# Kernel tuning notes

Measured on AMD Instinct MI355X. Metric: run time of the kernel, lower is better.

## Reference

```python
import jax, jax.numpy as jnp
import numpy as np

B, N, M = 2, 2048, 2048
D = 1024          # query_dim == context_dim == inner_dim
H, DH = 16, 64    # heads, dim_head
SCALE = DH ** -0.5


def setup_inputs() -> dict:
    key = jax.random.key(0)
    ks = jax.random.split(key, 7)
    s = 0.02
    return {
        "x": jax.random.normal(ks[0], (B, N, D), jnp.float32),
        "context": jax.random.normal(ks[1], (B, M, D), jnp.float32),
        "Wq": jax.random.normal(ks[2], (D, H * DH), jnp.float32) * s,
        "Wk": jax.random.normal(ks[3], (D, H * DH), jnp.float32) * s,
        "Wv": jax.random.normal(ks[4], (D, H * DH), jnp.float32) * s,
        "Wo": jax.random.normal(ks[5], (H * DH, D), jnp.float32) * s,
        "bo": jax.random.normal(ks[6], (D,), jnp.float32) * s,
    }


def reference(x, context, Wq, Wk, Wv, Wo, bo):
    # Linear projections (bias-free, as in to_q/to_k/to_v)
    q = (x @ Wq).reshape(B, N, H, DH)        # [B,N,H,DH]
    k = (context @ Wk).reshape(B, M, H, DH)  # [B,M,H,DH]
    v = (context @ Wv).reshape(B, M, H, DH)
    # QK^T * scale, softmax over keys, then AV
    sim = jnp.einsum('bnhd,bmhd->bhnm', q, k) * SCALE  # [B,H,N,M]
    attn = jax.nn.softmax(sim, axis=-1)
    out = jnp.einsum('bhnm,bmhd->bnhd', attn, v)       # [B,N,H,DH]
    out = out.reshape(B, N, H * DH)
    return out @ Wo + bo  # to_out Linear; dropout=0 is identity
```

## Files before the change

kernel.cpp:

```cpp
#include <hip/hip_runtime.h>

#define B_  2
#define N_  2048
#define M_  2048
#define D_  1024
#define H_  16
#define DH_ 64

typedef __bf16 bf16x8 __attribute__((ext_vector_type(8)));
typedef __bf16 bf16x4 __attribute__((ext_vector_type(4)));
typedef short  short4v __attribute__((ext_vector_type(4)));
typedef float  f32x4  __attribute__((ext_vector_type(4)));

#define GAS(p) ((__attribute__((address_space(1))) void*)(p))
#define LAS(p) ((__attribute__((address_space(3))) void*)(p))

#define QPRESCALE 0.18033688011112042f

__device__ __forceinline__ unsigned short f2bf(float f) {
    unsigned int u = __builtin_bit_cast(unsigned int, f);
    u += 0x7fffu + ((u >> 16) & 1u);
    return (unsigned short)(u >> 16);
}

__global__ __launch_bounds__(256) void prep(
    const float* __restrict__ x, const float* __restrict__ ctx,
    const float* __restrict__ Wq, const float* __restrict__ Wk,
    const float* __restrict__ Wv, const float* __restrict__ Wo,
    unsigned short* __restrict__ xb, unsigned short* __restrict__ cb,
    unsigned short* __restrict__ WTbase)
{
    if (blockIdx.z == 4) {
        int blk = blockIdx.y * 32 + blockIdx.x;
        int stride = 1024 * 256;
        for (int i = blk * 256 + threadIdx.x; i < 2097152; i += stride) {
            const float4* src; unsigned short* dst; int j;
            if (i < 1048576) { src = (const float4*)x;   dst = xb; j = i; }
            else             { src = (const float4*)ctx; dst = cb; j = i - 1048576; }
            float4 v = src[j];
            ushort4 o = make_ushort4(f2bf(v.x), f2bf(v.y), f2bf(v.z), f2bf(v.w));
            *(ushort4*)(dst + 4*j) = o;
        }
        return;
    }
    const float* W = (blockIdx.z == 0) ? Wq : (blockIdx.z == 1) ? Wk
                    : (blockIdx.z == 2) ? Wv : Wo;
    unsigned short* WT = WTbase + (size_t)blockIdx.z * 1048576;
    __shared__ unsigned short t[32][33];
    int tx = threadIdx.x & 31, ty8 = threadIdx.x >> 5;
    int c = blockIdx.x * 32 + tx;
#pragma unroll
    for (int i = 0; i < 4; ++i) {
        int r = blockIdx.y * 32 + i*8 + ty8;
        t[i*8 + ty8][tx] = f2bf(W[(size_t)r * 1024 + c]);
    }
    __syncthreads();
    int c2 = blockIdx.y * 32 + tx;
#pragma unroll
    for (int i = 0; i < 4; ++i) {
        int r2 = blockIdx.x * 32 + i*8 + ty8;
        WT[(size_t)r2 * 1024 + c2] = t[tx][i*8 + ty8];
    }
}

__global__ __launch_bounds__(256) void gemm128(
    const unsigned short* __restrict__ xb,
    const unsigned short* __restrict__ cb,
    const unsigned short* __restrict__ wT,
    const unsigned short* __restrict__ aoA,
    unsigned short* __restrict__ qkv_out,
    const float* __restrict__ bo,
    float* __restrict__ outF,
    int base_mode)
{
    __shared__ __align__(16) unsigned short As[128*32];
    __shared__ __align__(16) unsigned short Bs[128*32];

    const int mode = base_mode + blockIdx.z;
    const unsigned short* Amat;
    const unsigned short* Bt;
    if (mode == 0)      { Amat = wT;               Bt = xb; }
    else if (mode == 1) { Amat = wT + 1048576;     Bt = cb; }
    else if (mode == 2) { Amat = cb;               Bt = wT + 2*1048576; }
    else                { Amat = wT + 3*1048576;   Bt = aoA; }

    const int tid = threadIdx.x;
    const int w = tid >> 6, l = tid & 63;
    const int quad = l >> 4, l16 = l & 15;
    const int wm = w & 1, wn = w >> 1;
    int row0, col0;
    if (mode == 2) { row0 = blockIdx.x * 128; col0 = blockIdx.y * 128; }
    else           { row0 = blockIdx.y * 128; col0 = blockIdx.x * 128; }

    f32x4 acc[4][4];
#pragma unroll
    for (int i = 0; i < 4; ++i)
#pragma unroll
        for (int j = 0; j < 4; ++j) acc[i][j] = (f32x4){0.f, 0.f, 0.f, 0.f};

    for (int k0 = 0; k0 < 1024; k0 += 32) {
        __syncthreads();
#pragma unroll
        for (int i = 0; i < 2; ++i) {
            int s = i*256 + w*64 + l;
            int m = s >> 2, c = s & 3;
            int cs = c ^ ((m >> 1) & 3);
            __builtin_amdgcn_global_load_lds(
                GAS(Amat + (size_t)(row0 + m)*1024 + k0 + cs*8),
                LAS(As + (i*256 + w*64)*8), 16, 0, 0);
            __builtin_amdgcn_global_load_lds(
                GAS(Bt + (size_t)(col0 + m)*1024 + k0 + cs*8),
                LAS(Bs + (i*256 + w*64)*8), 16, 0, 0);
        }
        __syncthreads();

        bf16x8 af[4], bfr[4];
#pragma unroll
        for (int mt = 0; mt < 4; ++mt) {
            int m = wm*64 + mt*16 + l16;
            af[mt] = *reinterpret_cast<const bf16x8*>(As + m*32 + (quad ^ ((m >> 1) & 3))*8);
            int n = wn*64 + mt*16 + l16;
            bfr[mt] = *reinterpret_cast<const bf16x8*>(Bs + n*32 + (quad ^ ((n >> 1) & 3))*8);
        }
#pragma unroll
        for (int mt = 0; mt < 4; ++mt)
#pragma unroll
            for (int nt = 0; nt < 4; ++nt)
                acc[mt][nt] = __builtin_amdgcn_mfma_f32_16x16x32_bf16(
                    af[mt], bfr[nt], acc[mt][nt], 0, 0, 0);
    }

    if (mode == 3) {
#pragma unroll
        for (int mt = 0; mt < 4; ++mt) {
            int c = row0 + wm*64 + mt*16 + quad*4;
            float4 bv = *(const float4*)(bo + c);
#pragma unroll
            for (int nt = 0; nt < 4; ++nt) {
                int n = col0 + wn*64 + nt*16 + l16;
                float4 ov = make_float4(acc[mt][nt][0] + bv.x, acc[mt][nt][1] + bv.y,
                                        acc[mt][nt][2] + bv.z, acc[mt][nt][3] + bv.w);
                *(float4*)(outF + (size_t)n*1024 + c) = ov;
            }
        }
    } else if (mode == 2) {
#pragma unroll
        for (int mt = 0; mt < 4; ++mt) {
            int gr = row0 + wm*64 + mt*16 + quad*4;
            int b = gr >> 11, nidx = gr & 2047;
#pragma unroll
            for (int nt = 0; nt < 4; ++nt) {
                int col = col0 + wn*64 + nt*16 + l16;
                int h = col >> 6, d = col & 63;
                ushort4 pk = make_ushort4(f2bf(acc[mt][nt][0]), f2bf(acc[mt][nt][1]),
                                          f2bf(acc[mt][nt][2]), f2bf(acc[mt][nt][3]));
                *(ushort4*)(qkv_out + (size_t)2*4194304
                            + (size_t)((b*16 + h)*64 + d)*2048 + nidx) = pk;
            }
        }
    } else {
        const float qs = (mode == 0) ? QPRESCALE : 1.0f;
        unsigned short* obase = qkv_out + (size_t)mode*4194304;
#pragma unroll
        for (int nt = 0; nt < 4; ++nt) {
            int n = col0 + wn*64 + nt*16 + l16;
            int b = n >> 11, nidx = n & 2047;
#pragma unroll
            for (int mt = 0; mt < 4; ++mt) {
                int c = row0 + wm*64 + mt*16 + quad*4;
                int h = c >> 6, d = c & 63;
                ushort4 pkv = make_ushort4(
                    f2bf(acc[mt][nt][0] * qs), f2bf(acc[mt][nt][1] * qs),
                    f2bf(acc[mt][nt][2] * qs), f2bf(acc[mt][nt][3] * qs));
                *(ushort4*)(obase + (size_t)((b*16 + h)*2048 + nidx)*64 + d) = pkv;
            }
        }
    }
}

__global__ __launch_bounds__(256, 2) void flash_attn(
    const unsigned short* __restrict__ qw,
    const unsigned short* __restrict__ kw,
    const unsigned short* __restrict__ vtw,
    unsigned short* __restrict__ ao)
{
    __shared__ __align__(16) unsigned short Tile[2][9216];

    const int tid = threadIdx.x;
    const int w = tid >> 6, l = tid & 63;
    const int quad = l >> 4, l16 = l & 15;
    const int bh = blockIdx.z * H_ + blockIdx.y;
    const int q0 = blockIdx.x * 128 + w * 32;

    int goff[5];
#pragma unroll
    for (int i = 0; i < 5; ++i) {
        int n = i*256 + w*64 + l;
        int m = (n < 576) ? n : n - 576;
        int row = m / 9, c = m % 9;  if (c > 7) c = 7;
        goff[i] = (n < 576) ? row*64 + c*8 : row*2048 + c*8;
    }
    const unsigned short* kbase = kw + (size_t)bh*131072;
    const unsigned short* vbase = vtw + (size_t)bh*131072;

    bf16x8 qf[2][2];
#pragma unroll
    for (int qg = 0; qg < 2; ++qg)
#pragma unroll
        for (int s = 0; s < 2; ++s)
            qf[qg][s] = *reinterpret_cast<const bf16x8*>(
                qw + (size_t)(bh*2048 + q0 + qg*16 + l16)*64 + s*32 + quad*8);

    f32x4 accO[2][4];
#pragma unroll
    for (int qg = 0; qg < 2; ++qg)
#pragma unroll
        for (int td = 0; td < 4; ++td) accO[qg][td] = (f32x4){0.f, 0.f, 0.f, 0.f};
    float lpart[2] = {0.f, 0.f};

    const f32x4 zz = (f32x4){0.f, 0.f, 0.f, 0.f};

    {
#pragma unroll
        for (int i = 0; i < 4; ++i) {
            const unsigned short* bp = (i*4 + w < 9) ? kbase : vbase;
            __builtin_amdgcn_global_load_lds(GAS(bp + goff[i]),
                LAS(&Tile[0][(i*256 + w*64)*8]), 16, 0, 0);
        }
        if (w < 2)
            __builtin_amdgcn_global_load_lds(GAS(vbase + goff[4]),
                LAS(&Tile[0][(1024 + w*64)*8]), 16, 0, 0);
    }

    for (int it = 0; it < 32; ++it) {
        __syncthreads();
        const int cur = it & 1;

        if (it + 1 < 32) {
            const unsigned short* kp = kbase + (it+1)*4096;
            const unsigned short* vp = vbase + (it+1)*64;
#pragma unroll
            for (int i = 0; i < 4; ++i) {
                const unsigned short* bp = (i*4 + w < 9) ? kp : vp;
                __builtin_amdgcn_global_load_lds(GAS(bp + goff[i]),
                    LAS(&Tile[cur^1][(i*256 + w*64)*8]), 16, 0, 0);
            }
            if (w < 2)
                __builtin_amdgcn_global_load_lds(GAS(vp + goff[4]),
                    LAS(&Tile[cur^1][(1024 + w*64)*8]), 16, 0, 0);
        }

        const unsigned short* Ks = &Tile[cur][0];
        const unsigned short* Vs = &Tile[cur][4608];

        f32x4 sac[2][4];
#pragma unroll
        for (int t = 0; t < 4; ++t) {
            const unsigned short* krow = Ks + (t*16 + l16)*72 + quad*8;
            bf16x8 kf0 = *reinterpret_cast<const bf16x8*>(krow);
            bf16x8 kf1 = *reinterpret_cast<const bf16x8*>(krow + 32);
            sac[0][t] = __builtin_amdgcn_mfma_f32_16x16x32_bf16(kf0, qf[0][0], zz, 0, 0, 0);
            sac[1][t] = __builtin_amdgcn_mfma_f32_16x16x32_bf16(kf0, qf[1][0], zz, 0, 0, 0);
            sac[0][t] = __builtin_amdgcn_mfma_f32_16x16x32_bf16(kf1, qf[0][1], sac[0][t], 0, 0, 0);
            sac[1][t] = __builtin_amdgcn_mfma_f32_16x16x32_bf16(kf1, qf[1][1], sac[1][t], 0, 0, 0);
        }

        short4v pk[2][4];
#pragma unroll
        for (int qg = 0; qg < 2; ++qg) {
            float s0 = 0.f, s1 = 0.f, s2 = 0.f, s3 = 0.f;
#pragma unroll
            for (int t = 0; t < 4; ++t) {
                float p0 = __builtin_amdgcn_exp2f(sac[qg][t][0]);
                float p1 = __builtin_amdgcn_exp2f(sac[qg][t][1]);
                float p2 = __builtin_amdgcn_exp2f(sac[qg][t][2]);
                float p3 = __builtin_amdgcn_exp2f(sac[qg][t][3]);
                s0 += p0; s1 += p1; s2 += p2; s3 += p3;
                bf16x4 pb;
                pb[0] = (__bf16)p0; pb[1] = (__bf16)p1;
                pb[2] = (__bf16)p2; pb[3] = (__bf16)p3;
                pk[qg][t] = __builtin_bit_cast(short4v, pb);
            }
            lpart[qg] += (s0 + s1) + (s2 + s3);
        }

#pragma unroll
        for (int td = 0; td < 4; ++td) {
            const unsigned short* vrow = Vs + (td*16 + l16)*72 + quad*4;
#pragma unroll
            for (int t = 0; t < 4; ++t) {
                short4v vf = *reinterpret_cast<const short4v*>(vrow + t*16);
                accO[0][td] = __builtin_amdgcn_mfma_f32_16x16x16bf16_1k(
                    vf, pk[0][t], accO[0][td], 0, 0, 0);
                accO[1][td] = __builtin_amdgcn_mfma_f32_16x16x16bf16_1k(
                    vf, pk[1][t], accO[1][td], 0, 0, 0);
            }
        }
    }

#pragma unroll
    for (int qg = 0; qg < 2; ++qg) {
        float s = lpart[qg];
        s += __shfl_xor(s, 16);
        s += __shfl_xor(s, 32);
        float inv = 1.f / s;
        const size_t rowbase =
            (size_t)(blockIdx.z*2048 + q0 + qg*16 + l16)*1024 + blockIdx.y*64;
#pragma unroll
        for (int td = 0; td < 4; ++td)
#pragma unroll
            for (int r = 0; r < 4; ++r)
                ao[rowbase + td*16 + quad*4 + r] = f2bf(accO[qg][td][r] * inv);
    }
}

extern "C" void kernel_launch(void* const* d_in, const int* in_sizes, int n_in,
                              void* d_out, int out_size, void* d_ws, size_t ws_size,
                              hipStream_t stream)
{
    const float* x   = (const float*)d_in[0];
    const float* ctx = (const float*)d_in[1];
    const float* Wq  = (const float*)d_in[2];
    const float* Wk  = (const float*)d_in[3];
    const float* Wv  = (const float*)d_in[4];
    const float* Wo  = (const float*)d_in[5];
    const float* bo  = (const float*)d_in[6];
    float* out = (float*)d_out;

    unsigned short* ws  = (unsigned short*)d_ws;
    unsigned short* xb  = ws;
    unsigned short* cb  = ws + 4194304;
    unsigned short* wT  = ws + 8388608;
    unsigned short* qkv = ws + 12582912;
    unsigned short* ao  = ws;

    prep<<<dim3(32, 32, 5), dim3(256), 0, stream>>>(x, ctx, Wq, Wk, Wv, Wo, xb, cb, wT);
    gemm128<<<dim3(32, 8, 3), dim3(256), 0, stream>>>(xb, cb, wT, ao, qkv, bo, out, 0);
    flash_attn<<<dim3(16, 16, 2), dim3(256), 0, stream>>>(qkv, qkv + 4194304, qkv + 8388608, ao);
    gemm128<<<dim3(32, 8, 1), dim3(256), 0, stream>>>(xb, cb, wT, ao, qkv, bo, out, 3);
}
```

Measured before the change: 205.3 us.

## Split attention over key halves and merge partial outputs in a separate kernel

The flash attention kernel now splits the 2048 keys into two halves processed by separate blocks. This doubles the grid and raises launch bounds to 4 blocks per CU for better occupancy and latency hiding. Each half writes its unnormalized bf16 output and its row sums. A new merge kernel adds the two halves and normalizes. The cost is an extra launch, extra global traffic for the partials, and a second bf16 rounding of unnormalized values.

```diff
diff --git a/kernel.cpp b/kernel.cpp
--- a/kernel.cpp
+++ b/kernel.cpp
@@ -178,19 +178,22 @@
     }
 }
 
-__global__ __launch_bounds__(256, 2) void flash_attn(
+__global__ __launch_bounds__(256, 4) void flash_attn(
     const unsigned short* __restrict__ qw,
     const unsigned short* __restrict__ kw,
     const unsigned short* __restrict__ vtw,
-    unsigned short* __restrict__ ao)
+    unsigned short* __restrict__ oh,
+    float* __restrict__ ls)
 {
     __shared__ __align__(16) unsigned short Tile[2][9216];
 
     const int tid = threadIdx.x;
     const int w = tid >> 6, l = tid & 63;
     const int quad = l >> 4, l16 = l & 15;
-    const int bh = blockIdx.z * H_ + blockIdx.y;
+    const int b = blockIdx.z >> 1, half = blockIdx.z & 1;
+    const int bh = b * H_ + blockIdx.y;
     const int q0 = blockIdx.x * 128 + w * 32;
+    const int it0 = half * 16;
 
     int goff[5];
 #pragma unroll
@@ -221,22 +224,24 @@
     const f32x4 zz = (f32x4){0.f, 0.f, 0.f, 0.f};
 
     {
+        const unsigned short* kp = kbase + it0*4096;
+        const unsigned short* vp = vbase + it0*64;
 #pragma unroll
         for (int i = 0; i < 4; ++i) {
-            const unsigned short* bp = (i*4 + w < 9) ? kbase : vbase;
+            const unsigned short* bp = (i*4 + w < 9) ? kp : vp;
             __builtin_amdgcn_global_load_lds(GAS(bp + goff[i]),
                 LAS(&Tile[0][(i*256 + w*64)*8]), 16, 0, 0);
         }
         if (w < 2)
-            __builtin_amdgcn_global_load_lds(GAS(vbase + goff[4]),
+            __builtin_amdgcn_global_load_lds(GAS(vp + goff[4]),
                 LAS(&Tile[0][(1024 + w*64)*8]), 16, 0, 0);
     }
 
-    for (int it = 0; it < 32; ++it) {
+    for (int it = it0; it < it0 + 16; ++it) {
         __syncthreads();
         const int cur = it & 1;
 
-        if (it + 1 < 32) {
+        if (it + 1 < it0 + 16) {
             const unsigned short* kp = kbase + (it+1)*4096;
             const unsigned short* vp = vbase + (it+1)*64;
 #pragma unroll
@@ -298,20 +303,50 @@
         }
     }
 
+    unsigned short* ob = oh + (size_t)half*4194304;
 #pragma unroll
     for (int qg = 0; qg < 2; ++qg) {
         float s = lpart[qg];
         s += __shfl_xor(s, 16);
         s += __shfl_xor(s, 32);
-        float inv = 1.f / s;
-        const size_t rowbase =
-            (size_t)(blockIdx.z*2048 + q0 + qg*16 + l16)*1024 + blockIdx.y*64;
+        int q = q0 + qg*16 + l16;
+        if (quad == 0)
+            ls[half*65536 + bh*2048 + q] = s;
+        const size_t rowbase = (size_t)(b*2048 + q)*1024 + blockIdx.y*64;
 #pragma unroll
         for (int td = 0; td < 4; ++td)
 #pragma unroll
             for (int r = 0; r < 4; ++r)
-                ao[rowbase + td*16 + quad*4 + r] = f2bf(accO[qg][td][r] * inv);
-    }
+                ob[rowbase + td*16 + quad*4 + r] = f2bf(accO[qg][td][r]);
+    }
+}
+
+__global__ __launch_bounds__(256) void merge_halves(
+    unsigned short* __restrict__ o,
+    const float* __restrict__ ls)
+{
+    int t = blockIdx.x * 256 + threadIdx.x;
+    size_t flat = (size_t)t * 8;
+    int b = (int)(flat >> 21);
+    int rem = (int)(flat & 2097151);
+    int n = rem >> 10, c = rem & 1023, h = c >> 6;
+    int lidx = (b*16 + h)*2048 + n;
+    float inv = 1.f / (ls[lidx] + ls[65536 + lidx]);
+    uint4 a = *(const uint4*)(o + flat);
+    uint4 bv = *(const uint4*)(o + 4194304 + flat);
+    const unsigned int* au = (const unsigned int*)&a;
+    const unsigned int* bu = (const unsigned int*)&bv;
+    unsigned int outw[4];
+#pragma unroll
+    for (int i = 0; i < 4; ++i) {
+        unsigned int xx = au[i], yy = bu[i];
+        float lo = __builtin_bit_cast(float, (xx & 0xFFFFu) << 16)
+                 + __builtin_bit_cast(float, (yy & 0xFFFFu) << 16);
+        float hi = __builtin_bit_cast(float, xx & 0xFFFF0000u)
+                 + __builtin_bit_cast(float, yy & 0xFFFF0000u);
+        outw[i] = (unsigned int)f2bf(lo * inv) | ((unsigned int)f2bf(hi * inv) << 16);
+    }
+    *(uint4*)(o + flat) = *(uint4*)outw;
 }
 
 extern "C" void kernel_launch(void* const* d_in, const int* in_sizes, int n_in,
@@ -332,10 +367,13 @@
     unsigned short* cb  = ws + 4194304;
     unsigned short* wT  = ws + 8388608;
     unsigned short* qkv = ws + 12582912;
+    float* lsum = (float*)(ws + 25165824);
     unsigned short* ao  = ws;
 
     prep<<<dim3(32, 32, 5), dim3(256), 0, stream>>>(x, ctx, Wq, Wk, Wv, Wo, xb, cb, wT);
     gemm128<<<dim3(32, 8, 3), dim3(256), 0, stream>>>(xb, cb, wT, ao, qkv, bo, out, 0);
-    flash_attn<<<dim3(16, 16, 2), dim3(256), 0, stream>>>(qkv, qkv + 4194304, qkv + 8388608, ao);
+    flash_attn<<<dim3(16, 16, 4), dim3(256), 0, stream>>>(
+        qkv, qkv + 4194304, qkv + 8388608, ao, lsum);
+    merge_halves<<<dim3(2048), dim3(256), 0, stream>>>(ao, lsum);
     gemm128<<<dim3(32, 8, 1), dim3(256), 0, stream>>>(xb, cb, wT, ao, qkv, bo, out, 3);
 }
```

New measurement: 213.6 us. 4.0% more time.
